# Kernel tuning notes

Measured on AMD Instinct MI355X. Metric: run time of the kernel, lower is better.

## Reference

```python
import jax, jax.numpy as jnp
import numpy as np


def setup_inputs() -> dict:
    key = jax.random.key(0)
    k1, k2, k3, k4 = jax.random.split(key, 4)
    b, s, h, z = 4, 4096, 2048, 64
    scale = 1.0 / np.sqrt(h)
    return {
        "hidden_states": jax.random.normal(k1, (b, s, h), dtype=jnp.float32),
        # nn.Linear(h, z, bias=False): store as (h, z) so y = x @ W
        "Wq": jax.random.normal(k2, (h, z), dtype=jnp.float32) * scale,
        "Wk": jax.random.normal(k3, (h, z), dtype=jnp.float32) * scale,
        "Wv": jax.random.normal(k4, (h, z), dtype=jnp.float32) * scale,
    }


def reference(hidden_states, Wq, Wk, Wv):
    b, s, h = hidden_states.shape
    z = Wq.shape[1]
    # Three small projections: (b, s, z), cast to float32 as in original
    q = jnp.einsum("bsh,hz->bsz", hidden_states, Wq).astype(jnp.float32)
    k = jnp.einsum("bsh,hz->bsz", hidden_states, Wk).astype(jnp.float32)
    v = jnp.einsum("bsh,hz->bsz", hidden_states, Wv).astype(jnp.float32)
    # Per-token outer product over the expert dim: (b, s, z, z)
    attn = q[..., :, None] * k[..., None, :]
    attn = jax.nn.softmax(attn, axis=-1)
    # Weighted sum over the key expert axis j: out[..., i] = sum_j attn[..., i, j] * v[..., j]
    out = jnp.einsum("bsij,bsj->bsi", attn, v)
    return out.reshape(b * s, z)
```

## Files before the change

### kernel.cpp

```cpp
#include <hip/hip_runtime.h>


typedef __bf16 bf16x8 __attribute__((ext_vector_type(8)));
typedef float f32x4  __attribute__((ext_vector_type(4)));

#define NTOK   16384
#define HDIM   2048
#define NCHUNK 64
#define KCH    32
#define CH_STRIDE (12 * 2 * 512)

__global__ void pack_w_kernel(const float* __restrict__ Wq,
                              const float* __restrict__ Wk,
                              const float* __restrict__ Wv,
                              __bf16* __restrict__ bfrag)
{
  int u = blockIdx.x * blockDim.x + threadIdx.x;
  if (u >= NCHUNK * 12 * 64) return;
  int l  = u & 63;
  int tn = (u >> 6) % 12;
  int c  = u / (12 * 64);
  int n  = tn * 16 + (l & 15);
  int kb = c * 32 + ((l >> 4) << 3);
  const float* W = (n < 64) ? Wq : (n < 128) ? Wk : Wv;
  int nn = n & 63;
  bf16x8 hi, lo;
#pragma unroll
  for (int j = 0; j < 8; ++j) {
    float f = W[(size_t)(kb + j) * 64 + nn];
    __bf16 h = (__bf16)f;
    hi[j] = h;
    lo[j] = (__bf16)(f - (float)h);
  }
  size_t base = (size_t)(c * 12 + tn) * 1024 + (size_t)l * 8;
  *(bf16x8*)(bfrag + base)       = hi;
  *(bf16x8*)(bfrag + base + 512) = lo;
}

__global__ __launch_bounds__(512, 4) void router_kernel(
    const float* __restrict__ x,
    const __bf16* __restrict__ bfrag,
    float* __restrict__ out)
{
  const int tok0 = blockIdx.x * 32;
  const int w    = threadIdx.x >> 6;
  const int lane = threadIdx.x & 63;
  const int kh   = w >> 2;
  const int wc   = w & 3;
  const int mr   = lane & 15;
  const int quad = lane >> 4;

  __shared__ float qkv[2][32 * 196];

  const float*  a0 = x + (size_t)(tok0 + mr) * HDIM + quad * 8 + kh * 1024;
  const float*  a1 = a0 + 16 * HDIM;
  const __bf16* bp = bfrag + (size_t)(kh * KCH) * CH_STRIDE
                           + (size_t)(3 * wc) * 1024 + (size_t)lane * 8;

  f32x4 acc[2][3];
#pragma unroll
  for (int i = 0; i < 2; ++i)
#pragma unroll
    for (int t = 0; t < 3; ++t)
      acc[i][t] = (f32x4){0.f, 0.f, 0.f, 0.f};

  float4 pA[4];
  bf16x8 pBh[3], pBl[3];
  pA[0] = *(const float4*)(a0);
  pA[1] = *(const float4*)(a0 + 4);
  pA[2] = *(const float4*)(a1);
  pA[3] = *(const float4*)(a1 + 4);
#pragma unroll
  for (int t = 0; t < 3; ++t) {
    pBh[t] = *(const bf16x8*)(bp + (size_t)t * 1024);
    pBl[t] = *(const bf16x8*)(bp + (size_t)t * 1024 + 512);
  }

  for (int c = 0; c < KCH; ++c) {
    float4 A[4]; bf16x8 Bh[3], Bl[3];
#pragma unroll
    for (int i = 0; i < 4; ++i) A[i] = pA[i];
#pragma unroll
    for (int t = 0; t < 3; ++t) { Bh[t] = pBh[t]; Bl[t] = pBl[t]; }

    if (c + 1 < KCH) {
      const float*  na0 = a0 + (c + 1) * 32;
      const float*  na1 = a1 + (c + 1) * 32;
      const __bf16* nbp = bp + (size_t)(c + 1) * CH_STRIDE;
      pA[0] = *(const float4*)(na0);
      pA[1] = *(const float4*)(na0 + 4);
      pA[2] = *(const float4*)(na1);
      pA[3] = *(const float4*)(na1 + 4);
#pragma unroll
      for (int t = 0; t < 3; ++t) {
        pBh[t] = *(const bf16x8*)(nbp + (size_t)t * 1024);
        pBl[t] = *(const bf16x8*)(nbp + (size_t)t * 1024 + 512);
      }
    }

    bf16x8 ah[2], al[2];
#pragma unroll
    for (int i = 0; i < 2; ++i) {
      float av[8] = {A[2*i].x, A[2*i].y, A[2*i].z, A[2*i].w,
                     A[2*i+1].x, A[2*i+1].y, A[2*i+1].z, A[2*i+1].w};
#pragma unroll
      for (int j = 0; j < 8; ++j) {
        __bf16 h = (__bf16)av[j];
        ah[i][j] = h;
        al[i][j] = (__bf16)(av[j] - (float)h);
      }
    }

#pragma unroll
    for (int i = 0; i < 2; ++i)
#pragma unroll
      for (int t = 0; t < 3; ++t) {
        acc[i][t] = __builtin_amdgcn_mfma_f32_16x16x32_bf16(ah[i], Bh[t], acc[i][t], 0, 0, 0);
        acc[i][t] = __builtin_amdgcn_mfma_f32_16x16x32_bf16(al[i], Bh[t], acc[i][t], 0, 0, 0);
        acc[i][t] = __builtin_amdgcn_mfma_f32_16x16x32_bf16(ah[i], Bl[t], acc[i][t], 0, 0, 0);
      }
  }

#pragma unroll
  for (int i = 0; i < 2; ++i)
#pragma unroll
    for (int t = 0; t < 3; ++t) {
      int col = wc * 48 + t * 16 + mr;
      int row = i * 16 + quad * 4;
#pragma unroll
      for (int r = 0; r < 4; ++r)
        qkv[kh][(row + r) * 196 + col] = acc[i][t][r];
    }
  __syncthreads();

  const int tt = threadIdx.x >> 4;
  const int g  = threadIdx.x & 15;
  const float* q0 = qkv[0] + tt * 196;
  const float* q1 = qkv[1] + tt * 196;
  float qs[4], lsum[4], osum[4];
#pragma unroll
  for (int ii = 0; ii < 4; ++ii) {
    qs[ii]   = (q0[g * 4 + ii] + q1[g * 4 + ii]) * 1.44269504f;
    lsum[ii] = 0.f;
    osum[ii] = 0.f;
  }
  for (int j = 0; j < 64; ++j) {
    float kj = q0[64 + j]  + q1[64 + j];
    float vj = q0[128 + j] + q1[128 + j];
#pragma unroll
    for (int ii = 0; ii < 4; ++ii) {
      float e = __builtin_amdgcn_exp2f(qs[ii] * kj);
      lsum[ii] += e;
      osum[ii] = fmaf(e, vj, osum[ii]);
    }
  }
  float4 r0;
  r0.x = osum[0] / lsum[0]; r0.y = osum[1] / lsum[1];
  r0.z = osum[2] / lsum[2]; r0.w = osum[3] / lsum[3];
  float* op = out + (size_t)(tok0 + tt) * 64 + g * 4;
  *(float4*)op = r0;
}

extern "C" void kernel_launch(void* const* d_in, const int* in_sizes, int n_in,
                              void* d_out, int out_size, void* d_ws, size_t ws_size,
                              hipStream_t stream)
{
  const float* x  = (const float*)d_in[0];
  const float* Wq = (const float*)d_in[1];
  const float* Wk = (const float*)d_in[2];
  const float* Wv = (const float*)d_in[3];
  __bf16* bfrag   = (__bf16*)d_ws;
  float*  out     = (float*)d_out;

  pack_w_kernel<<<(NCHUNK * 12 * 64 + 255) / 256, 256, 0, stream>>>(Wq, Wk, Wv, bfrag);
  router_kernel<<<NTOK / 32, 512, 0, stream>>>(x, bfrag, out);
}
```

Before: 267.5 us.

## Stage activation tiles through LDS with async global_load_lds double buffering

Activation loads change from per-lane register prefetch to direct global-to-LDS async copies (global_load_lds, 16 bytes) into a double-buffered, XOR-swizzled shared tile. Each wave then reads its MFMA operands from LDS. The goal is fully coalesced, deduplicated A loads, less register pressure, and overlap of the next chunk's copy with the current chunk's MFMAs. In exchange it adds a block-wide __syncthreads per K chunk, and B fragments are no longer prefetched, so they are loaded synchronously each iteration.

Measured after the change: 241.1 us. 1.11x faster.

```diff
diff --git a/kernel.cpp b/kernel.cpp
--- a/kernel.cpp
+++ b/kernel.cpp
@@ -9,6 +9,13 @@
 #define NCHUNK 64
 #define KCH    32
 #define CH_STRIDE (12 * 2 * 512)
+
+#define SWZ(row, kq) ((kq) ^ ((row) & 7))
+
+#define GLOAD_LDS16(g, l)                                                      \
+  __builtin_amdgcn_global_load_lds(                                            \
+      (const __attribute__((address_space(1))) void*)(g),                      \
+      (__attribute__((address_space(3))) void*)(l), 16, 0, 0)
 
 __global__ void pack_w_kernel(const float* __restrict__ Wq,
                               const float* __restrict__ Wk,
@@ -51,9 +58,16 @@
   const int quad = lane >> 4;
 
   __shared__ float qkv[2][32 * 196];
+  __shared__ float bufA[2][2][1024];
 
-  const float*  a0 = x + (size_t)(tok0 + mr) * HDIM + quad * 8 + kh * 1024;
-  const float*  a1 = a0 + 16 * HDIM;
+  const int su   = threadIdx.x & 255;
+  const int srow = su >> 3;
+  const int skq  = su & 7;
+  const float* aSrc = x + (size_t)(tok0 + srow) * HDIM + kh * 1024
+                        + SWZ(srow, skq) * 4;
+  float* aDst0 = &bufA[kh][0][(w & 3) * 256];
+  float* aDst1 = &bufA[kh][1][(w & 3) * 256];
+
   const __bf16* bp = bfrag + (size_t)(kh * KCH) * CH_STRIDE
                            + (size_t)(3 * wc) * 1024 + (size_t)lane * 8;
 
@@ -64,39 +78,31 @@
     for (int t = 0; t < 3; ++t)
       acc[i][t] = (f32x4){0.f, 0.f, 0.f, 0.f};
 
-  float4 pA[4];
-  bf16x8 pBh[3], pBl[3];
-  pA[0] = *(const float4*)(a0);
-  pA[1] = *(const float4*)(a0 + 4);
-  pA[2] = *(const float4*)(a1);
-  pA[3] = *(const float4*)(a1 + 4);
-#pragma unroll
-  for (int t = 0; t < 3; ++t) {
-    pBh[t] = *(const bf16x8*)(bp + (size_t)t * 1024);
-    pBl[t] = *(const bf16x8*)(bp + (size_t)t * 1024 + 512);
-  }
+  GLOAD_LDS16(aSrc, aDst0);
+  __syncthreads();
 
   for (int c = 0; c < KCH; ++c) {
-    float4 A[4]; bf16x8 Bh[3], Bl[3];
+    if (c + 1 < KCH) {
+      const float* s = aSrc + (c + 1) * 32;
+      if (c & 1) GLOAD_LDS16(s, aDst0);
+      else       GLOAD_LDS16(s, aDst1);
+    }
+
+    const __bf16* cbp = bp + (size_t)c * CH_STRIDE;
+    bf16x8 Bh[3], Bl[3];
 #pragma unroll
-    for (int i = 0; i < 4; ++i) A[i] = pA[i];
-#pragma unroll
-    for (int t = 0; t < 3; ++t) { Bh[t] = pBh[t]; Bl[t] = pBl[t]; }
+    for (int t = 0; t < 3; ++t) {
+      Bh[t] = *(const bf16x8*)(cbp + (size_t)t * 1024);
+      Bl[t] = *(const bf16x8*)(cbp + (size_t)t * 1024 + 512);
+    }
 
-    if (c + 1 < KCH) {
-      const float*  na0 = a0 + (c + 1) * 32;
-      const float*  na1 = a1 + (c + 1) * 32;
-      const __bf16* nbp = bp + (size_t)(c + 1) * CH_STRIDE;
-      pA[0] = *(const float4*)(na0);
-      pA[1] = *(const float4*)(na0 + 4);
-      pA[2] = *(const float4*)(na1);
-      pA[3] = *(const float4*)(na1 + 4);
-#pragma unroll
-      for (int t = 0; t < 3; ++t) {
-        pBh[t] = *(const bf16x8*)(nbp + (size_t)t * 1024);
-        pBl[t] = *(const bf16x8*)(nbp + (size_t)t * 1024 + 512);
-      }
-    }
+    const float* ab = bufA[kh][c & 1];
+    const int r0 = mr, r1 = 16 + mr;
+    float4 A[4];
+    A[0] = *(const float4*)&ab[r0 * 32 + SWZ(r0, 2 * quad)     * 4];
+    A[1] = *(const float4*)&ab[r0 * 32 + SWZ(r0, 2 * quad + 1) * 4];
+    A[2] = *(const float4*)&ab[r1 * 32 + SWZ(r1, 2 * quad)     * 4];
+    A[3] = *(const float4*)&ab[r1 * 32 + SWZ(r1, 2 * quad + 1) * 4];
 
     bf16x8 ah[2], al[2];
 #pragma unroll
@@ -119,6 +125,8 @@
         acc[i][t] = __builtin_amdgcn_mfma_f32_16x16x32_bf16(al[i], Bh[t], acc[i][t], 0, 0, 0);
         acc[i][t] = __builtin_amdgcn_mfma_f32_16x16x32_bf16(ah[i], Bl[t], acc[i][t], 0, 0, 0);
       }
+
+    __syncthreads();
   }
 
 #pragma unroll
@@ -154,11 +162,11 @@
       osum[ii] = fmaf(e, vj, osum[ii]);
     }
   }
-  float4 r0;
-  r0.x = osum[0] / lsum[0]; r0.y = osum[1] / lsum[1];
-  r0.z = osum[2] / lsum[2]; r0.w = osum[3] / lsum[3];
+  float4 r0v;
+  r0v.x = osum[0] / lsum[0]; r0v.y = osum[1] / lsum[1];
+  r0v.z = osum[2] / lsum[2]; r0v.w = osum[3] / lsum[3];
   float* op = out + (size_t)(tok0 + tt) * 64 + g * 4;
-  *(float4*)op = r0;
+  *(float4*)op = r0v;
 }
 
 extern "C" void kernel_launch(void* const* d_in, const int* in_sizes, int n_in,
```
